# Optimization experiments

Hardware: AMD Instinct MI355X
Metric: run time of the kernel (lower is better)

## Reference

```python
import jax, jax.numpy as jnp
import numpy as np

B, D, C = 32, 30, 4        # batch, input spatial, in-channels
KS = 3                     # kernel size per dim
OD = D - KS + 1            # 28 (valid padding, stride 1)
P = OD ** 3                # 21952 output positions
K = (KS ** 3) * C          # 108 taps per output position
F = 4                      # output filters


def _patches(x):
    # x: [B, D, D, D, C] -> [B, P, K]
    xt = jnp.transpose(x, (0, 4, 1, 2, 3))  # NCDHW
    p = jax.lax.conv_general_dilated_patches(
        xt, filter_shape=(KS, KS, KS), window_strides=(1, 1, 1), padding='VALID')
    # p: [B, C*KS^3, OD, OD, OD]
    p = jnp.transpose(p, (0, 2, 3, 4, 1))
    return p.reshape(p.shape[0], P, K)


def _local_conv(x, W):
    # Locally-connected 3D conv (unshared weights) == structured sparse matmul.
    # W: [P, K, F] one weight per (output position, tap, filter).
    return jnp.einsum('bpk,pkf->bpf', _patches(x), W)


def setup_inputs() -> dict:
    key = jax.random.key(0)
    ks = jax.random.split(key, 7)
    x = jax.random.normal(ks[0], (B, D, D, D, C), jnp.float32)
    kernel_loc = jax.random.normal(ks[1], (P, K, F), jnp.float32) * 0.05
    kernel_rho = jax.random.normal(ks[2], (P, K, F), jnp.float32) * 0.1 - 5.0  # softplus -> small scale
    bias = jax.random.normal(ks[3], (F,), jnp.float32) * 0.05
    eps = jax.random.normal(ks[4], (P, K, F), jnp.float32)
    sign_in = jax.random.rademacher(ks[5], (B, D, D, D, C), jnp.float32)
    sign_out = jax.random.rademacher(ks[6], (B, P, F), jnp.float32)
    return dict(x=x, kernel_loc=kernel_loc, kernel_rho=kernel_rho, bias=bias,
                eps=eps, sign_in=sign_in, sign_out=sign_out)


def reference(x, kernel_loc, kernel_rho, bias, eps, sign_in, sign_out):
    # Flipout estimator: deterministic mean path + sign-perturbed noise path.
    scale = jax.nn.softplus(kernel_rho)
    out = _local_conv(x, kernel_loc)                                  # [B, P, F]
    out = out + sign_out * _local_conv(x * sign_in, scale * eps)      # flipout perturbation
    out = out + bias                                                  # per-filter bias (channels_last)
    return out.reshape(x.shape[0], OD, OD, OD, F)
```

## Files before the change

kernel.cpp:

```cpp
#include <hip/hip_runtime.h>


constexpr int Bn   = 32;
constexpr int Dn   = 30;
constexpr int Cn   = 4;
constexpr int ODn  = 28;
constexpr int Pn   = ODn * ODn * ODn;
constexpr int Tt   = 27;
constexpr int Kn   = Tt * Cn;
constexpr int PPB  = 16;
constexpr int THREADS = 256;
constexpr int WSTRIDE = Kn + 1;

__device__ __forceinline__ unsigned bf16rne(float f) {
    unsigned u = __float_as_uint(f);
    return (u + 0x7fffu + ((u >> 16) & 1u)) >> 16;
}
__device__ __forceinline__ float bflo(unsigned u) { return __uint_as_float(u << 16); }
__device__ __forceinline__ float bfhi(unsigned u) { return __uint_as_float(u & 0xffff0000u); }

__global__ __launch_bounds__(THREADS) void lc3d_flipout_kernel(
    const float* __restrict__ x,
    const float* __restrict__ loc,
    const float* __restrict__ rho,
    const float* __restrict__ bias,
    const float* __restrict__ eps,
    const float* __restrict__ sgn_in,
    const float* __restrict__ sgn_out,
    float* __restrict__ out)
{
    __shared__ uint4 w[PPB * WSTRIDE];

    const int tid    = threadIdx.x;
    const int p_base = blockIdx.x * PPB;

    const float4* loc4 = (const float4*)loc + (size_t)p_base * Kn;
    const float4* rho4 = (const float4*)rho + (size_t)p_base * Kn;
    const float4* eps4 = (const float4*)eps + (size_t)p_base * Kn;

    for (int g = tid; g < PPB * Kn; g += THREADS) {
        const int pl = g / Kn;
        const int k  = g - pl * Kn;
        const float4 L = loc4[g];
        const float4 R = rho4[g];
        const float4 E = eps4[g];
        float nx = (R.x > 15.f ? R.x : __logf(1.f + __expf(R.x))) * E.x;
        float ny = (R.y > 15.f ? R.y : __logf(1.f + __expf(R.y))) * E.y;
        float nz = (R.z > 15.f ? R.z : __logf(1.f + __expf(R.z))) * E.z;
        float nw = (R.w > 15.f ? R.w : __logf(1.f + __expf(R.w))) * E.w;
        uint4 pk;
        pk.x = bf16rne(L.x) | (bf16rne(L.y) << 16);
        pk.y = bf16rne(L.z) | (bf16rne(L.w) << 16);
        pk.z = bf16rne(nx)  | (bf16rne(ny) << 16);
        pk.w = bf16rne(nz)  | (bf16rne(nw) << 16);
        w[pl * WSTRIDE + k] = pk;
    }
    __syncthreads();

    const int pl = tid & 15;
    const int bh = tid >> 4;
    const int b0 = bh, b1 = bh + 16;
    const int p  = p_base + pl;
    const int od   = p / (ODn * ODn);
    const int prem = p - od * (ODn * ODn);
    const int oh   = prem / ODn;
    const int ow   = prem - oh * ODn;

    const float4* x4 = (const float4*)x;
    const float4* s4 = (const float4*)sgn_in;
    const size_t v0 = (((size_t)b0 * Dn + od) * Dn + oh) * Dn + ow;
    const size_t v1 = (((size_t)b1 * Dn + od) * Dn + oh) * Dn + ow;
    const uint4* wp = w + pl * WSTRIDE;

    float a00=0.f,a01=0.f,a02=0.f,a03=0.f;
    float a10=0.f,a11=0.f,a12=0.f,a13=0.f;
    float n00=0.f,n01=0.f,n02=0.f,n03=0.f;
    float n10=0.f,n11=0.f,n12=0.f,n13=0.f;

#define CHAN(c, xa_c, sa_c, xb_c, sb_c)                                      \
    {                                                                        \
        const uint4 wv = wp[(c) * Tt + t];                                   \
        const float m0 = bflo(wv.x), m1 = bfhi(wv.x);                        \
        const float m2 = bflo(wv.y), m3 = bfhi(wv.y);                        \
        const float q0 = bflo(wv.z), q1 = bfhi(wv.z);                        \
        const float q2 = bflo(wv.w), q3 = bfhi(wv.w);                        \
        a00 = fmaf(xa_c, m0, a00); a01 = fmaf(xa_c, m1, a01);                \
        a02 = fmaf(xa_c, m2, a02); a03 = fmaf(xa_c, m3, a03);                \
        a10 = fmaf(xb_c, m0, a10); a11 = fmaf(xb_c, m1, a11);                \
        a12 = fmaf(xb_c, m2, a12); a13 = fmaf(xb_c, m3, a13);                \
        const float ya = (xa_c) * (sa_c);                                    \
        const float yb = (xb_c) * (sb_c);                                    \
        n00 = fmaf(ya, q0, n00); n01 = fmaf(ya, q1, n01);                    \
        n02 = fmaf(ya, q2, n02); n03 = fmaf(ya, q3, n03);                    \
        n10 = fmaf(yb, q0, n10); n11 = fmaf(yb, q1, n11);                    \
        n12 = fmaf(yb, q2, n12); n13 = fmaf(yb, q3, n13);                    \
    }

    #pragma unroll
    for (int kd = 0; kd < 3; ++kd) {
        #pragma unroll
        for (int kh = 0; kh < 3; ++kh) {
            const int roff = (kd * Dn + kh) * Dn;
            const float4* xr0 = x4 + v0 + roff;
            const float4* sr0 = s4 + v0 + roff;
            const float4* xr1 = x4 + v1 + roff;
            const float4* sr1 = s4 + v1 + roff;
            #pragma unroll
            for (int kw = 0; kw < 3; ++kw) {
                const int t = (kd * 3 + kh) * 3 + kw;
                const float4 xa = xr0[kw];
                const float4 sa = sr0[kw];
                const float4 xb = xr1[kw];
                const float4 sb = sr1[kw];
                CHAN(0, xa.x, sa.x, xb.x, sb.x);
                CHAN(1, xa.y, sa.y, xb.y, sb.y);
                CHAN(2, xa.z, sa.z, xb.z, sb.z);
                CHAN(3, xa.w, sa.w, xb.w, sb.w);
            }
        }
    }
#undef CHAN

    const float4 bi = *(const float4*)bias;
    const size_t ob0 = (size_t)b0 * Pn + p;
    const size_t ob1 = (size_t)b1 * Pn + p;
    const float4 so0 = ((const float4*)sgn_out)[ob0];
    const float4 so1 = ((const float4*)sgn_out)[ob1];
    float4 o0, o1;
    o0.x = fmaf(so0.x, n00, a00) + bi.x;
    o0.y = fmaf(so0.y, n01, a01) + bi.y;
    o0.z = fmaf(so0.z, n02, a02) + bi.z;
    o0.w = fmaf(so0.w, n03, a03) + bi.w;
    o1.x = fmaf(so1.x, n10, a10) + bi.x;
    o1.y = fmaf(so1.y, n11, a11) + bi.y;
    o1.z = fmaf(so1.z, n12, a12) + bi.z;
    o1.w = fmaf(so1.w, n13, a13) + bi.w;
    ((float4*)out)[ob0] = o0;
    ((float4*)out)[ob1] = o1;
}

extern "C" void kernel_launch(void* const* d_in, const int* in_sizes, int n_in,
                              void* d_out, int out_size, void* d_ws, size_t ws_size,
                              hipStream_t stream) {
    const float* x    = (const float*)d_in[0];
    const float* loc  = (const float*)d_in[1];
    const float* rho  = (const float*)d_in[2];
    const float* bias = (const float*)d_in[3];
    const float* eps  = (const float*)d_in[4];
    const float* si   = (const float*)d_in[5];
    const float* so   = (const float*)d_in[6];
    float* out = (float*)d_out;

    lc3d_flipout_kernel<<<dim3(Pn / PPB), dim3(THREADS), 0, stream>>>(
        x, loc, rho, bias, eps, si, so, out);
}
```

Baseline: 217.5 us.

## Split into weight pack pass and main kernel with transposed bf16 weight layout

```diff
diff --git a/kernel.cpp b/kernel.cpp
--- a/kernel.cpp
+++ b/kernel.cpp
@@ -8,9 +8,9 @@
 constexpr int Pn   = ODn * ODn * ODn;
 constexpr int Tt   = 27;
 constexpr int Kn   = Tt * Cn;
-constexpr int PPB  = 16;
-constexpr int THREADS = 256;
-constexpr int WSTRIDE = Kn + 1;
+constexpr int PT   = 64;
+constexpr int NPT  = Pn / PT;
+constexpr size_t WS_NEED = (size_t)Pn * Kn * 16;
 
 __device__ __forceinline__ unsigned bf16rne(float f) {
     unsigned u = __float_as_uint(f);
@@ -19,28 +19,155 @@
 __device__ __forceinline__ float bflo(unsigned u) { return __uint_as_float(u << 16); }
 __device__ __forceinline__ float bfhi(unsigned u) { return __uint_as_float(u & 0xffff0000u); }
 
-__global__ __launch_bounds__(THREADS) void lc3d_flipout_kernel(
-    const float* __restrict__ x,
-    const float* __restrict__ loc,
-    const float* __restrict__ rho,
+__global__ __launch_bounds__(256) void lc3d_pack(
+    const float4* __restrict__ loc4,
+    const float4* __restrict__ rho4,
+    const float4* __restrict__ eps4,
+    uint4* __restrict__ w)
+{
+    __shared__ uint4 lds[Tt * 66];
+    const int pt = blockIdx.x;
+    const int c  = blockIdx.y;
+    const int p_base = pt * PT;
+    const int tid = threadIdx.x;
+
+    for (int g = tid; g < PT * Tt; g += 256) {
+        const int t     = g % Tt;
+        const int p_loc = g / Tt;
+        const size_t src = (size_t)(p_base + p_loc) * Kn + c * Tt + t;
+        const float4 L = loc4[src];
+        const float4 R = rho4[src];
+        const float4 E = eps4[src];
+        float nx = (R.x > 15.f ? R.x : __logf(1.f + __expf(R.x))) * E.x;
+        float ny = (R.y > 15.f ? R.y : __logf(1.f + __expf(R.y))) * E.y;
+        float nz = (R.z > 15.f ? R.z : __logf(1.f + __expf(R.z))) * E.z;
+        float nw = (R.w > 15.f ? R.w : __logf(1.f + __expf(R.w))) * E.w;
+        uint4 pk;
+        pk.x = bf16rne(L.x) | (bf16rne(L.y) << 16);
+        pk.y = bf16rne(L.z) | (bf16rne(L.w) << 16);
+        pk.z = bf16rne(nx)  | (bf16rne(ny) << 16);
+        pk.w = bf16rne(nz)  | (bf16rne(nw) << 16);
+        lds[t * 66 + p_loc] = pk;
+    }
+    __syncthreads();
+
+    for (int g = tid; g < PT * Tt; g += 256) {
+        const int p_loc = g & 63;
+        const int t     = g >> 6;
+        w[((size_t)pt * Kn + t * 4 + c) * PT + p_loc] = lds[t * 66 + p_loc];
+    }
+}
+
+__global__ __launch_bounds__(256) void lc3d_main(
+    const uint4* __restrict__ w,
+    const float4* __restrict__ x4,
+    const float4* __restrict__ s4,
     const float* __restrict__ bias,
-    const float* __restrict__ eps,
-    const float* __restrict__ sgn_in,
-    const float* __restrict__ sgn_out,
-    float* __restrict__ out)
+    const float4* __restrict__ so4,
+    float4* __restrict__ out4)
 {
-    __shared__ uint4 w[PPB * WSTRIDE];
-
-    const int tid    = threadIdx.x;
+    const int tid = threadIdx.x;
+    const int pl  = tid & 63;
+    const int bh  = tid >> 6;
+    const int pt  = blockIdx.x;
+    const int bg  = blockIdx.y;
+    const int p   = pt * PT + pl;
+    const int b0  = bg * 8 + bh * 2;
+    const int b1  = b0 + 1;
+
+    const int od   = p / (ODn * ODn);
+    const int prem = p - od * (ODn * ODn);
+    const int oh   = prem / ODn;
+    const int ow   = prem - oh * ODn;
+
+    const size_t v0 = (((size_t)b0 * Dn + od) * Dn + oh) * Dn + ow;
+    const size_t v1 = (((size_t)b1 * Dn + od) * Dn + oh) * Dn + ow;
+    const uint4* wp = w + (size_t)pt * (Kn * PT) + pl;
+
+    float a00=0.f,a01=0.f,a02=0.f,a03=0.f;
+    float a10=0.f,a11=0.f,a12=0.f,a13=0.f;
+    float n00=0.f,n01=0.f,n02=0.f,n03=0.f;
+    float n10=0.f,n11=0.f,n12=0.f,n13=0.f;
+
+#define CHAN(WV, xa_c, sa_c, xb_c, sb_c)                                     \
+    {                                                                        \
+        const float m0 = bflo(WV.x), m1 = bfhi(WV.x);                        \
+        const float m2 = bflo(WV.y), m3 = bfhi(WV.y);                        \
+        const float q0 = bflo(WV.z), q1 = bfhi(WV.z);                        \
+        const float q2 = bflo(WV.w), q3 = bfhi(WV.w);                        \
+        a00 = fmaf(xa_c, m0, a00); a01 = fmaf(xa_c, m1, a01);                \
+        a02 = fmaf(xa_c, m2, a02); a03 = fmaf(xa_c, m3, a03);                \
+        a10 = fmaf(xb_c, m0, a10); a11 = fmaf(xb_c, m1, a11);                \
+        a12 = fmaf(xb_c, m2, a12); a13 = fmaf(xb_c, m3, a13);                \
+        const float ya = (xa_c) * (sa_c);                                    \
+        const float yb = (xb_c) * (sb_c);                                    \
+        n00 = fmaf(ya, q0, n00); n01 = fmaf(ya, q1, n01);                    \
+        n02 = fmaf(ya, q2, n02); n03 = fmaf(ya, q3, n03);                    \
+        n10 = fmaf(yb, q0, n10); n11 = fmaf(yb, q1, n11);                    \
+        n12 = fmaf(yb, q2, n12); n13 = fmaf(yb, q3, n13);                    \
+    }
+
+    #pragma unroll
+    for (int kd = 0; kd < 3; ++kd) {
+        #pragma unroll
+        for (int kh = 0; kh < 3; ++kh) {
+            #pragma unroll
+            for (int kw = 0; kw < 3; ++kw) {
+                const int t    = (kd * 3 + kh) * 3 + kw;
+                const int roff = (kd * Dn + kh) * Dn + kw;
+                const float4 xa = x4[v0 + roff];
+                const float4 sa = s4[v0 + roff];
+                const float4 xb = x4[v1 + roff];
+                const float4 sb = s4[v1 + roff];
+                const uint4 w0 = wp[(t * 4 + 0) * PT];
+                const uint4 w1 = wp[(t * 4 + 1) * PT];
+                const uint4 w2 = wp[(t * 4 + 2) * PT];
+                const uint4 w3 = wp[(t * 4 + 3) * PT];
+                CHAN(w0, xa.x, sa.x, xb.x, sb.x);
+                CHAN(w1, xa.y, sa.y, xb.y, sb.y);
+                CHAN(w2, xa.z, sa.z, xb.z, sb.z);
+                CHAN(w3, xa.w, sa.w, xb.w, sb.w);
+            }
+        }
+    }
+#undef CHAN
+
+    const float4 bi = *(const float4*)bias;
+    const size_t ob0 = (size_t)b0 * Pn + p;
+    const size_t ob1 = (size_t)b1 * Pn + p;
+    const float4 so0 = so4[ob0];
+    const float4 so1 = so4[ob1];
+    float4 o0, o1;
+    o0.x = fmaf(so0.x, n00, a00) + bi.x;
+    o0.y = fmaf(so0.y, n01, a01) + bi.y;
+    o0.z = fmaf(so0.z, n02, a02) + bi.z;
+    o0.w = fmaf(so0.w, n03, a03) + bi.w;
+    o1.x = fmaf(so1.x, n10, a10) + bi.x;
+    o1.y = fmaf(so1.y, n11, a11) + bi.y;
+    o1.z = fmaf(so1.z, n12, a12) + bi.z;
+    o1.w = fmaf(so1.w, n13, a13) + bi.w;
+    out4[ob0] = o0;
+    out4[ob1] = o1;
+}
+
+constexpr int PPB = 16;
+constexpr int WSTRIDE = Kn + 1;
+
+__global__ __launch_bounds__(256) void lc3d_flipout_kernel(
+    const float* __restrict__ x, const float* __restrict__ loc,
+    const float* __restrict__ rho, const float* __restrict__ bias,
+    const float* __restrict__ eps, const float* __restrict__ sgn_in,
+    const float* __restrict__ sgn_out, float* __restrict__ out)
+{
+    __shared__ uint4 wsh[PPB * WSTRIDE];
+    const int tid = threadIdx.x;
     const int p_base = blockIdx.x * PPB;
-
     const float4* loc4 = (const float4*)loc + (size_t)p_base * Kn;
     const float4* rho4 = (const float4*)rho + (size_t)p_base * Kn;
     const float4* eps4 = (const float4*)eps + (size_t)p_base * Kn;
-
-    for (int g = tid; g < PPB * Kn; g += THREADS) {
-        const int pl = g / Kn;
-        const int k  = g - pl * Kn;
+    for (int g = tid; g < PPB * Kn; g += 256) {
+        const int plc = g / Kn;
+        const int k   = g - plc * Kn;
         const float4 L = loc4[g];
         const float4 R = rho4[g];
         const float4 E = eps4[g];
@@ -53,30 +180,24 @@
         pk.y = bf16rne(L.z) | (bf16rne(L.w) << 16);
         pk.z = bf16rne(nx)  | (bf16rne(ny) << 16);
         pk.w = bf16rne(nz)  | (bf16rne(nw) << 16);
-        w[pl * WSTRIDE + k] = pk;
+        wsh[plc * WSTRIDE + k] = pk;
     }
     __syncthreads();
-
     const int pl = tid & 15;
     const int bh = tid >> 4;
     const int b0 = bh, b1 = bh + 16;
     const int p  = p_base + pl;
-    const int od   = p / (ODn * ODn);
+    const int od = p / (ODn * ODn);
     const int prem = p - od * (ODn * ODn);
-    const int oh   = prem / ODn;
-    const int ow   = prem - oh * ODn;
-
+    const int oh = prem / ODn;
+    const int ow = prem - oh * ODn;
     const float4* x4 = (const float4*)x;
     const float4* s4 = (const float4*)sgn_in;
     const size_t v0 = (((size_t)b0 * Dn + od) * Dn + oh) * Dn + ow;
     const size_t v1 = (((size_t)b1 * Dn + od) * Dn + oh) * Dn + ow;
-    const uint4* wp = w + pl * WSTRIDE;
-
-    float a00=0.f,a01=0.f,a02=0.f,a03=0.f;
-    float a10=0.f,a11=0.f,a12=0.f,a13=0.f;
-    float n00=0.f,n01=0.f,n02=0.f,n03=0.f;
-    float n10=0.f,n11=0.f,n12=0.f,n13=0.f;
-
+    const uint4* wp = wsh + pl * WSTRIDE;
+    float a00=0.f,a01=0.f,a02=0.f,a03=0.f, a10=0.f,a11=0.f,a12=0.f,a13=0.f;
+    float n00=0.f,n01=0.f,n02=0.f,n03=0.f, n10=0.f,n11=0.f,n12=0.f,n13=0.f;
 #define CHAN(c, xa_c, sa_c, xb_c, sb_c)                                      \
     {                                                                        \
         const uint4 wv = wp[(c) * Tt + t];                                   \
@@ -95,32 +216,25 @@
         n10 = fmaf(yb, q0, n10); n11 = fmaf(yb, q1, n11);                    \
         n12 = fmaf(yb, q2, n12); n13 = fmaf(yb, q3, n13);                    \
     }
-
     #pragma unroll
-    for (int kd = 0; kd < 3; ++kd) {
+    for (int kd = 0; kd < 3; ++kd)
         #pragma unroll
         for (int kh = 0; kh < 3; ++kh) {
             const int roff = (kd * Dn + kh) * Dn;
-            const float4* xr0 = x4 + v0 + roff;
-            const float4* sr0 = s4 + v0 + roff;
-            const float4* xr1 = x4 + v1 + roff;
-            const float4* sr1 = s4 + v1 + roff;
             #pragma unroll
             for (int kw = 0; kw < 3; ++kw) {
                 const int t = (kd * 3 + kh) * 3 + kw;
-                const float4 xa = xr0[kw];
-                const float4 sa = sr0[kw];
-                const float4 xb = xr1[kw];
-                const float4 sb = sr1[kw];
+                const float4 xa = x4[v0 + roff + kw];
+                const float4 sa = s4[v0 + roff + kw];
+                const float4 xb = x4[v1 + roff + kw];
+                const float4 sb = s4[v1 + roff + kw];
                 CHAN(0, xa.x, sa.x, xb.x, sb.x);
                 CHAN(1, xa.y, sa.y, xb.y, sb.y);
                 CHAN(2, xa.z, sa.z, xb.z, sb.z);
                 CHAN(3, xa.w, sa.w, xb.w, sb.w);
             }
         }
-    }
 #undef CHAN
-
     const float4 bi = *(const float4*)bias;
     const size_t ob0 = (size_t)b0 * Pn + p;
     const size_t ob1 = (size_t)b1 * Pn + p;
@@ -151,6 +265,15 @@
     const float* so   = (const float*)d_in[6];
     float* out = (float*)d_out;
 
-    lc3d_flipout_kernel<<<dim3(Pn / PPB), dim3(THREADS), 0, stream>>>(
-        x, loc, rho, bias, eps, si, so, out);
-}
+    if (ws_size >= WS_NEED) {
+        uint4* w = (uint4*)d_ws;
+        lc3d_pack<<<dim3(NPT, 4), dim3(256), 0, stream>>>(
+            (const float4*)loc, (const float4*)rho, (const float4*)eps, w);
+        lc3d_main<<<dim3(NPT, 4), dim3(256), 0, stream>>>(
+            w, (const float4*)x, (const float4*)si, bias,
+            (const float4*)so, (float4*)out);
+    } else {
+        lc3d_flipout_kernel<<<dim3(Pn / PPB), dim3(256), 0, stream>>>(
+            x, loc, rho, bias, eps, si, so, out);
+    }
+}
```

Result: slower. 241.2 us (+10.9%).

## Double-buffer weight staging per kd slice to overlap loads with compute

Applied to the files above, without the earlier changes.

```diff
diff --git a/kernel.cpp b/kernel.cpp
--- a/kernel.cpp
+++ b/kernel.cpp
@@ -10,7 +10,10 @@
 constexpr int Kn   = Tt * Cn;
 constexpr int PPB  = 16;
 constexpr int THREADS = 256;
-constexpr int WSTRIDE = Kn + 1;
+constexpr int CHK  = 36;
+constexpr int NITEM = PPB * CHK;
+constexpr int WST  = 37;
+constexpr int BUFSZ = PPB * WST;
 
 __device__ __forceinline__ unsigned bf16rne(float f) {
     unsigned u = __float_as_uint(f);
@@ -18,6 +21,19 @@
 }
 __device__ __forceinline__ float bflo(unsigned u) { return __uint_as_float(u << 16); }
 __device__ __forceinline__ float bfhi(unsigned u) { return __uint_as_float(u & 0xffff0000u); }
+
+__device__ __forceinline__ uint4 packw(float4 L, float4 R, float4 E) {
+    float nx = (R.x > 15.f ? R.x : __logf(1.f + __expf(R.x))) * E.x;
+    float ny = (R.y > 15.f ? R.y : __logf(1.f + __expf(R.y))) * E.y;
+    float nz = (R.z > 15.f ? R.z : __logf(1.f + __expf(R.z))) * E.z;
+    float nw = (R.w > 15.f ? R.w : __logf(1.f + __expf(R.w))) * E.w;
+    uint4 pk;
+    pk.x = bf16rne(L.x) | (bf16rne(L.y) << 16);
+    pk.y = bf16rne(L.z) | (bf16rne(L.w) << 16);
+    pk.z = bf16rne(nx)  | (bf16rne(ny) << 16);
+    pk.w = bf16rne(nz)  | (bf16rne(nw) << 16);
+    return pk;
+}
 
 __global__ __launch_bounds__(THREADS) void lc3d_flipout_kernel(
     const float* __restrict__ x,
@@ -29,33 +45,27 @@
     const float* __restrict__ sgn_out,
     float* __restrict__ out)
 {
-    __shared__ uint4 w[PPB * WSTRIDE];
+    __shared__ uint4 wbuf[2][BUFSZ];
 
     const int tid    = threadIdx.x;
     const int p_base = blockIdx.x * PPB;
 
-    const float4* loc4 = (const float4*)loc + (size_t)p_base * Kn;
-    const float4* rho4 = (const float4*)rho + (size_t)p_base * Kn;
-    const float4* eps4 = (const float4*)eps + (size_t)p_base * Kn;
+    const float4* loc4 = (const float4*)loc;
+    const float4* rho4 = (const float4*)rho;
+    const float4* eps4 = (const float4*)eps;
 
-    for (int g = tid; g < PPB * Kn; g += THREADS) {
-        const int pl = g / Kn;
-        const int k  = g - pl * Kn;
-        const float4 L = loc4[g];
-        const float4 R = rho4[g];
-        const float4 E = eps4[g];
-        float nx = (R.x > 15.f ? R.x : __logf(1.f + __expf(R.x))) * E.x;
-        float ny = (R.y > 15.f ? R.y : __logf(1.f + __expf(R.y))) * E.y;
-        float nz = (R.z > 15.f ? R.z : __logf(1.f + __expf(R.z))) * E.z;
-        float nw = (R.w > 15.f ? R.w : __logf(1.f + __expf(R.w))) * E.w;
-        uint4 pk;
-        pk.x = bf16rne(L.x) | (bf16rne(L.y) << 16);
-        pk.y = bf16rne(L.z) | (bf16rne(L.w) << 16);
-        pk.z = bf16rne(nx)  | (bf16rne(ny) << 16);
-        pk.w = bf16rne(nz)  | (bf16rne(nw) << 16);
-        w[pl * WSTRIDE + k] = pk;
+    const int g0 = tid, g1 = tid + THREADS, g2 = tid + 2 * THREADS;
+    int s0, d0, s1, d1, s2 = 0, d2 = 0;
+    {
+        int pl = g0 / CHK, r = g0 - pl * CHK, c = r / 9, j = r - c * 9;
+        s0 = (p_base + pl) * Kn + c * Tt + j;  d0 = pl * WST + r;
+        pl = g1 / CHK; r = g1 - pl * CHK; c = r / 9; j = r - c * 9;
+        s1 = (p_base + pl) * Kn + c * Tt + j;  d1 = pl * WST + r;
+        if (tid < 64) {
+            pl = g2 / CHK; r = g2 - pl * CHK; c = r / 9; j = r - c * 9;
+            s2 = (p_base + pl) * Kn + c * Tt + j;  d2 = pl * WST + r;
+        }
     }
-    __syncthreads();
 
     const int pl = tid & 15;
     const int bh = tid >> 4;
@@ -70,20 +80,27 @@
     const float4* s4 = (const float4*)sgn_in;
     const size_t v0 = (((size_t)b0 * Dn + od) * Dn + oh) * Dn + ow;
     const size_t v1 = (((size_t)b1 * Dn + od) * Dn + oh) * Dn + ow;
-    const uint4* wp = w + pl * WSTRIDE;
 
     float a00=0.f,a01=0.f,a02=0.f,a03=0.f;
     float a10=0.f,a11=0.f,a12=0.f,a13=0.f;
     float n00=0.f,n01=0.f,n02=0.f,n03=0.f;
     float n10=0.f,n11=0.f,n12=0.f,n13=0.f;
 
-#define CHAN(c, xa_c, sa_c, xb_c, sb_c)                                      \
+    float4 L0 = loc4[s0], R0 = rho4[s0], E0 = eps4[s0];
+    float4 L1 = loc4[s1], R1 = rho4[s1], E1 = eps4[s1];
+    float4 L2, R2, E2;
+    if (tid < 64) { L2 = loc4[s2]; R2 = rho4[s2]; E2 = eps4[s2]; }
+    wbuf[0][d0] = packw(L0, R0, E0);
+    wbuf[0][d1] = packw(L1, R1, E1);
+    if (tid < 64) wbuf[0][d2] = packw(L2, R2, E2);
+    __syncthreads();
+
+#define CHAN(WV, xa_c, sa_c, xb_c, sb_c)                                     \
     {                                                                        \
-        const uint4 wv = wp[(c) * Tt + t];                                   \
-        const float m0 = bflo(wv.x), m1 = bfhi(wv.x);                        \
-        const float m2 = bflo(wv.y), m3 = bfhi(wv.y);                        \
-        const float q0 = bflo(wv.z), q1 = bfhi(wv.z);                        \
-        const float q2 = bflo(wv.w), q3 = bfhi(wv.w);                        \
+        const float m0 = bflo(WV.x), m1 = bfhi(WV.x);                        \
+        const float m2 = bflo(WV.y), m3 = bfhi(WV.y);                        \
+        const float q0 = bflo(WV.z), q1 = bfhi(WV.z);                        \
+        const float q2 = bflo(WV.w), q3 = bfhi(WV.w);                        \
         a00 = fmaf(xa_c, m0, a00); a01 = fmaf(xa_c, m1, a01);                \
         a02 = fmaf(xa_c, m2, a02); a03 = fmaf(xa_c, m3, a03);                \
         a10 = fmaf(xb_c, m0, a10); a11 = fmaf(xb_c, m1, a11);                \
@@ -98,25 +115,41 @@
 
     #pragma unroll
     for (int kd = 0; kd < 3; ++kd) {
+        if (kd < 2) {
+            const int o = (kd + 1) * 9;
+            L0 = loc4[s0 + o]; R0 = rho4[s0 + o]; E0 = eps4[s0 + o];
+            L1 = loc4[s1 + o]; R1 = rho4[s1 + o]; E1 = eps4[s1 + o];
+            if (tid < 64) { L2 = loc4[s2 + o]; R2 = rho4[s2 + o]; E2 = eps4[s2 + o]; }
+        }
+
+        const uint4* wp = wbuf[kd & 1] + pl * WST;
         #pragma unroll
         for (int kh = 0; kh < 3; ++kh) {
-            const int roff = (kd * Dn + kh) * Dn;
-            const float4* xr0 = x4 + v0 + roff;
-            const float4* sr0 = s4 + v0 + roff;
-            const float4* xr1 = x4 + v1 + roff;
-            const float4* sr1 = s4 + v1 + roff;
             #pragma unroll
             for (int kw = 0; kw < 3; ++kw) {
-                const int t = (kd * 3 + kh) * 3 + kw;
-                const float4 xa = xr0[kw];
-                const float4 sa = sr0[kw];
-                const float4 xb = xr1[kw];
-                const float4 sb = sr1[kw];
-                CHAN(0, xa.x, sa.x, xb.x, sb.x);
-                CHAN(1, xa.y, sa.y, xb.y, sb.y);
-                CHAN(2, xa.z, sa.z, xb.z, sb.z);
-                CHAN(3, xa.w, sa.w, xb.w, sb.w);
+                const int tl   = kh * 3 + kw;
+                const int roff = (kd * Dn + kh) * Dn + kw;
+                const float4 xa = x4[v0 + roff];
+                const float4 sa = s4[v0 + roff];
+                const float4 xb = x4[v1 + roff];
+                const float4 sb = s4[v1 + roff];
+                const uint4 w0 = wp[0 * 9 + tl];
+                const uint4 w1 = wp[1 * 9 + tl];
+                const uint4 w2 = wp[2 * 9 + tl];
+                const uint4 w3 = wp[3 * 9 + tl];
+                CHAN(w0, xa.x, sa.x, xb.x, sb.x);
+                CHAN(w1, xa.y, sa.y, xb.y, sb.y);
+                CHAN(w2, xa.z, sa.z, xb.z, sb.z);
+                CHAN(w3, xa.w, sa.w, xb.w, sb.w);
             }
+        }
+
+        if (kd < 2) {
+            uint4* nb = wbuf[(kd + 1) & 1];
+            nb[d0] = packw(L0, R0, E0);
+            nb[d1] = packw(L1, R1, E1);
+            if (tid < 64) nb[d2] = packw(L2, R2, E2);
+            __syncthreads();
         }
     }
 #undef CHAN
```

After: 477.8 us. +119.7%, slower.

## Use persistent grid with XCD-aware tile mapping for L2 locality

Applied to the files above, without the earlier changes.

```diff
diff --git a/kernel.cpp b/kernel.cpp
--- a/kernel.cpp
+++ b/kernel.cpp
@@ -9,8 +9,10 @@
 constexpr int Tt   = 27;
 constexpr int Kn   = Tt * Cn;
 constexpr int PPB  = 16;
+constexpr int NT   = Pn / PPB;
 constexpr int THREADS = 256;
 constexpr int WSTRIDE = Kn + 1;
+constexpr int GRID = 1280;
 
 __device__ __forceinline__ unsigned bf16rne(float f) {
     unsigned u = __float_as_uint(f);
@@ -29,114 +31,116 @@
     const float* __restrict__ sgn_out,
     float* __restrict__ out)
 {
-    __shared__ uint4 w[PPB * WSTRIDE];
+    __shared__ uint4 wsh[PPB * WSTRIDE];
 
-    const int tid    = threadIdx.x;
-    const int p_base = blockIdx.x * PPB;
+    const int tid = threadIdx.x;
 
-    const float4* loc4 = (const float4*)loc + (size_t)p_base * Kn;
-    const float4* rho4 = (const float4*)rho + (size_t)p_base * Kn;
-    const float4* eps4 = (const float4*)eps + (size_t)p_base * Kn;
+    const int xcd  = blockIdx.x & 7;
+    const int slot = blockIdx.x >> 3;
+    const int Nx = (xcd < 4) ? 172 : 171;
+    const int Tx = (xcd < 4) ? xcd * 172 : 688 + (xcd - 4) * 171;
+    const int ntiles = (slot + 160 < Nx) ? 2 : 1;
 
-    for (int g = tid; g < PPB * Kn; g += THREADS) {
-        const int pl = g / Kn;
-        const int k  = g - pl * Kn;
-        const float4 L = loc4[g];
-        const float4 R = rho4[g];
-        const float4 E = eps4[g];
-        float nx = (R.x > 15.f ? R.x : __logf(1.f + __expf(R.x))) * E.x;
-        float ny = (R.y > 15.f ? R.y : __logf(1.f + __expf(R.y))) * E.y;
-        float nz = (R.z > 15.f ? R.z : __logf(1.f + __expf(R.z))) * E.z;
-        float nw = (R.w > 15.f ? R.w : __logf(1.f + __expf(R.w))) * E.w;
-        uint4 pk;
-        pk.x = bf16rne(L.x) | (bf16rne(L.y) << 16);
-        pk.y = bf16rne(L.z) | (bf16rne(L.w) << 16);
-        pk.z = bf16rne(nx)  | (bf16rne(ny) << 16);
-        pk.w = bf16rne(nz)  | (bf16rne(nw) << 16);
-        w[pl * WSTRIDE + k] = pk;
-    }
-    __syncthreads();
+    for (int it = 0; it < ntiles; ++it) {
+        const int p_base = (Tx + slot + it * 160) * PPB;
+        if (it) __syncthreads();
 
-    const int pl = tid & 15;
-    const int bh = tid >> 4;
-    const int b0 = bh, b1 = bh + 16;
-    const int p  = p_base + pl;
-    const int od   = p / (ODn * ODn);
-    const int prem = p - od * (ODn * ODn);
-    const int oh   = prem / ODn;
-    const int ow   = prem - oh * ODn;
+        const float4* loc4 = (const float4*)loc + (size_t)p_base * Kn;
+        const float4* rho4 = (const float4*)rho + (size_t)p_base * Kn;
+        const float4* eps4 = (const float4*)eps + (size_t)p_base * Kn;
+        for (int g = tid; g < PPB * Kn; g += THREADS) {
+            const int plc = g / Kn;
+            const int k   = g - plc * Kn;
+            const float4 L = loc4[g];
+            const float4 R = rho4[g];
+            const float4 E = eps4[g];
+            float nx = (R.x > 15.f ? R.x : __logf(1.f + __expf(R.x))) * E.x;
+            float ny = (R.y > 15.f ? R.y : __logf(1.f + __expf(R.y))) * E.y;
+            float nz = (R.z > 15.f ? R.z : __logf(1.f + __expf(R.z))) * E.z;
+            float nw = (R.w > 15.f ? R.w : __logf(1.f + __expf(R.w))) * E.w;
+            uint4 pk;
+            pk.x = bf16rne(L.x) | (bf16rne(L.y) << 16);
+            pk.y = bf16rne(L.z) | (bf16rne(L.w) << 16);
+            pk.z = bf16rne(nx)  | (bf16rne(ny) << 16);
+            pk.w = bf16rne(nz)  | (bf16rne(nw) << 16);
+            wsh[plc * WSTRIDE + k] = pk;
+        }
+        __syncthreads();
 
-    const float4* x4 = (const float4*)x;
-    const float4* s4 = (const float4*)sgn_in;
-    const size_t v0 = (((size_t)b0 * Dn + od) * Dn + oh) * Dn + ow;
-    const size_t v1 = (((size_t)b1 * Dn + od) * Dn + oh) * Dn + ow;
-    const uint4* wp = w + pl * WSTRIDE;
+        const int pl = tid & 15;
+        const int bh = tid >> 4;
+        const int b0 = bh, b1 = bh + 16;
+        const int p  = p_base + pl;
+        const int od = p / (ODn * ODn);
+        const int prem = p - od * (ODn * ODn);
+        const int oh = prem / ODn;
+        const int ow = prem - oh * ODn;
+        const float4* x4 = (const float4*)x;
+        const float4* s4 = (const float4*)sgn_in;
+        const size_t v0 = (((size_t)b0 * Dn + od) * Dn + oh) * Dn + ow;
+        const size_t v1 = (((size_t)b1 * Dn + od) * Dn + oh) * Dn + ow;
+        const uint4* wp = wsh + pl * WSTRIDE;
 
-    float a00=0.f,a01=0.f,a02=0.f,a03=0.f;
-    float a10=0.f,a11=0.f,a12=0.f,a13=0.f;
-    float n00=0.f,n01=0.f,n02=0.f,n03=0.f;
-    float n10=0.f,n11=0.f,n12=0.f,n13=0.f;
+        float a00=0.f,a01=0.f,a02=0.f,a03=0.f, a10=0.f,a11=0.f,a12=0.f,a13=0.f;
+        float n00=0.f,n01=0.f,n02=0.f,n03=0.f, n10=0.f,n11=0.f,n12=0.f,n13=0.f;
 
 #define CHAN(c, xa_c, sa_c, xb_c, sb_c)                                      \
-    {                                                                        \
-        const uint4 wv = wp[(c) * Tt + t];                                   \
-        const float m0 = bflo(wv.x), m1 = bfhi(wv.x);                        \
-        const float m2 = bflo(wv.y), m3 = bfhi(wv.y);                        \
-        const float q0 = bflo(wv.z), q1 = bfhi(wv.z);                        \
-        const float q2 = bflo(wv.w), q3 = bfhi(wv.w);                        \
-        a00 = fmaf(xa_c, m0, a00); a01 = fmaf(xa_c, m1, a01);                \
-        a02 = fmaf(xa_c, m2, a02); a03 = fmaf(xa_c, m3, a03);                \
-        a10 = fmaf(xb_c, m0, a10); a11 = fmaf(xb_c, m1, a11);                \
-        a12 = fmaf(xb_c, m2, a12); a13 = fmaf(xb_c, m3, a13);                \
-        const float ya = (xa_c) * (sa_c);                                    \
-        const float yb = (xb_c) * (sb_c);                                    \
-        n00 = fmaf(ya, q0, n00); n01 = fmaf(ya, q1, n01);                    \
-        n02 = fmaf(ya, q2, n02); n03 = fmaf(ya, q3, n03);                    \
-        n10 = fmaf(yb, q0, n10); n11 = fmaf(yb, q1, n11);                    \
-        n12 = fmaf(yb, q2, n12); n13 = fmaf(yb, q3, n13);                    \
-    }
+        {                                                                    \
+            const uint4 wv = wp[(c) * Tt + t];                               \
+            const float m0 = bflo(wv.x), m1 = bfhi(wv.x);                    \
+            const float m2 = bflo(wv.y), m3 = bfhi(wv.y);                    \
+            const float q0 = bflo(wv.z), q1 = bfhi(wv.z);                    \
+            const float q2 = bflo(wv.w), q3 = bfhi(wv.w);                    \
+            a00 = fmaf(xa_c, m0, a00); a01 = fmaf(xa_c, m1, a01);            \
+            a02 = fmaf(xa_c, m2, a02); a03 = fmaf(xa_c, m3, a03);            \
+            a10 = fmaf(xb_c, m0, a10); a11 = fmaf(xb_c, m1, a11);            \
+            a12 = fmaf(xb_c, m2, a12); a13 = fmaf(xb_c, m3, a13);            \
+            const float ya = (xa_c) * (sa_c);                                \
+            const float yb = (xb_c) * (sb_c);                                \
+            n00 = fmaf(ya, q0, n00); n01 = fmaf(ya, q1, n01);                \
+            n02 = fmaf(ya, q2, n02); n03 = fmaf(ya, q3, n03);                \
+            n10 = fmaf(yb, q0, n10); n11 = fmaf(yb, q1, n11);                \
+            n12 = fmaf(yb, q2, n12); n13 = fmaf(yb, q3, n13);                \
+        }
 
-    #pragma unroll
-    for (int kd = 0; kd < 3; ++kd) {
         #pragma unroll
-        for (int kh = 0; kh < 3; ++kh) {
-            const int roff = (kd * Dn + kh) * Dn;
-            const float4* xr0 = x4 + v0 + roff;
-            const float4* sr0 = s4 + v0 + roff;
-            const float4* xr1 = x4 + v1 + roff;
-            const float4* sr1 = s4 + v1 + roff;
+        for (int kd = 0; kd < 3; ++kd) {
             #pragma unroll
-            for (int kw = 0; kw < 3; ++kw) {
-                const int t = (kd * 3 + kh) * 3 + kw;
-                const float4 xa = xr0[kw];
-                const float4 sa = sr0[kw];
-                const float4 xb = xr1[kw];
-                const float4 sb = sr1[kw];
-                CHAN(0, xa.x, sa.x, xb.x, sb.x);
-                CHAN(1, xa.y, sa.y, xb.y, sb.y);
-                CHAN(2, xa.z, sa.z, xb.z, sb.z);
-                CHAN(3, xa.w, sa.w, xb.w, sb.w);
+            for (int kh = 0; kh < 3; ++kh) {
+                const int roff = (kd * Dn + kh) * Dn;
+                #pragma unroll
+                for (int kw = 0; kw < 3; ++kw) {
+                    const int t = (kd * 3 + kh) * 3 + kw;
+                    const float4 xa = x4[v0 + roff + kw];
+                    const float4 sa = s4[v0 + roff + kw];
+                    const float4 xb = x4[v1 + roff + kw];
+                    const float4 sb = s4[v1 + roff + kw];
+                    CHAN(0, xa.x, sa.x, xb.x, sb.x);
+                    CHAN(1, xa.y, sa.y, xb.y, sb.y);
+                    CHAN(2, xa.z, sa.z, xb.z, sb.z);
+                    CHAN(3, xa.w, sa.w, xb.w, sb.w);
+                }
             }
         }
-    }
 #undef CHAN
 
-    const float4 bi = *(const float4*)bias;
-    const size_t ob0 = (size_t)b0 * Pn + p;
-    const size_t ob1 = (size_t)b1 * Pn + p;
-    const float4 so0 = ((const float4*)sgn_out)[ob0];
-    const float4 so1 = ((const float4*)sgn_out)[ob1];
-    float4 o0, o1;
-    o0.x = fmaf(so0.x, n00, a00) + bi.x;
-    o0.y = fmaf(so0.y, n01, a01) + bi.y;
-    o0.z = fmaf(so0.z, n02, a02) + bi.z;
-    o0.w = fmaf(so0.w, n03, a03) + bi.w;
-    o1.x = fmaf(so1.x, n10, a10) + bi.x;
-    o1.y = fmaf(so1.y, n11, a11) + bi.y;
-    o1.z = fmaf(so1.z, n12, a12) + bi.z;
-    o1.w = fmaf(so1.w, n13, a13) + bi.w;
-    ((float4*)out)[ob0] = o0;
-    ((float4*)out)[ob1] = o1;
+        const float4 bi = *(const float4*)bias;
+        const size_t ob0 = (size_t)b0 * Pn + p;
+        const size_t ob1 = (size_t)b1 * Pn + p;
+        const float4 so0 = ((const float4*)sgn_out)[ob0];
+        const float4 so1 = ((const float4*)sgn_out)[ob1];
+        float4 o0, o1;
+        o0.x = fmaf(so0.x, n00, a00) + bi.x;
+        o0.y = fmaf(so0.y, n01, a01) + bi.y;
+        o0.z = fmaf(so0.z, n02, a02) + bi.z;
+        o0.w = fmaf(so0.w, n03, a03) + bi.w;
+        o1.x = fmaf(so1.x, n10, a10) + bi.x;
+        o1.y = fmaf(so1.y, n11, a11) + bi.y;
+        o1.z = fmaf(so1.z, n12, a12) + bi.z;
+        o1.w = fmaf(so1.w, n13, a13) + bi.w;
+        ((float4*)out)[ob0] = o0;
+        ((float4*)out)[ob1] = o1;
+    }
 }
 
 extern "C" void kernel_launch(void* const* d_in, const int* in_sizes, int n_in,
@@ -151,6 +155,6 @@
     const float* so   = (const float*)d_in[6];
     float* out = (float*)d_out;
 
-    lc3d_flipout_kernel<<<dim3(Pn / PPB), dim3(THREADS), 0, stream>>>(
+    lc3d_flipout_kernel<<<dim3(GRID), dim3(THREADS), 0, stream>>>(
         x, loc, rho, bias, eps, si, so, out);
 }
```

New measurement: 203.8 us. 6.3% less time.
